# Performance work log

Hardware: AMD Instinct MI355X
Metric: run time of the kernel (lower is better)

Reference implementation:

```python
import jax, jax.numpy as jnp
import numpy as np

MARGIN = 0.1   # init kwarg m
EPS = 1e-6     # CosineSimilarity eps
B, D, C = 8192, 1024, 14
LABEL_P = 0.1


def setup_inputs() -> dict:
    key = jax.random.key(0)
    k1, k2 = jax.random.split(key)
    pred = jax.random.normal(k1, (B, D), dtype=jnp.float32)
    gt = (jax.random.uniform(k2, (B, C)) < LABEL_P).astype(jnp.float32)
    return {"pred": pred, "gt": gt}


def _cos(x, y):
    # torch.nn.CosineSimilarity(dim=1, eps=1e-6): dot / max(||x||*||y||, eps)
    dot = jnp.sum(x * y, axis=1)
    nx = jnp.sqrt(jnp.sum(x * x, axis=1))
    ny = jnp.sqrt(jnp.sum(y * y, axis=1))
    return dot / jnp.maximum(nx * ny, EPS)


def reference(pred, gt):
    n = pred.shape[0]
    has = jnp.sum(gt, axis=1) > 0                      # [B] labeled rows (idxs_a)
    share = (gt @ gt.T) > 0                            # [B,B] rows sharing any label
    # Labeled anchor: positives = rows sharing a label (incl. self),
    #                 negatives = setdiff(idxs_a, rows_pos) U idxs_n == ~share row.
    # Unlabeled anchor: positives = unlabeled rows, negatives = labeled rows.
    pos_mask = jnp.where(has[:, None], share, ~has[None, :])
    neg_mask = jnp.where(has[:, None], ~share, has[None, :])
    # Uniform sampling among masked columns via Gumbel-max (replaces random.sample)
    kp, kn = jax.random.split(jax.random.key(42))
    NEG_INF = jnp.float32(-1e30)
    pos_idx = jnp.argmax(jnp.where(pos_mask, jax.random.gumbel(kp, (n, n)), NEG_INF), axis=1)
    neg_idx = jnp.argmax(jnp.where(neg_mask, jax.random.gumbel(kn, (n, n)), NEG_INF), axis=1)
    anchor = pred
    positive = pred[pos_idx]
    negative = pred[neg_idx]
    cos_v = _cos(anchor, positive) - _cos(anchor, negative) + MARGIN
    return jnp.mean(jnp.maximum(cos_v, 0.0))
```

## Files before the change

### kernel.cpp

```cpp
#include <hip/hip_runtime.h>
#include <hip/hip_bf16.h>
#include <stdint.h>

#define NB 8192
#define ND 1024
#define NC 14

#define ROTL(x, r) __builtin_amdgcn_alignbit((x), (x), 32u - (r))
#define ADD3_IMM(x, s, imm) \
  asm("v_add3_u32 %0, %1, %2, " #imm : "=v"(x) : "v"(x), "v"(s))

static inline uint32_t rotl32h(uint32_t x, int r) { return (x << r) | (x >> (32 - r)); }
static void tf2x32_host(uint32_t k0, uint32_t k1, uint32_t x0, uint32_t x1,
                        uint32_t* o0, uint32_t* o1) {
  uint32_t ks[3] = { k0, k1, k0 ^ k1 ^ 0x1BD11BDAu };
  static const int R[8] = {13, 15, 26, 6, 17, 29, 16, 24};
  x0 += k0; x1 += k1;
  for (int g = 0; g < 5; ++g) {
    const int* rr = (g & 1) ? (R + 4) : R;
    for (int i = 0; i < 4; ++i) { x0 += x1; x1 = rotl32h(x1, rr[i]); x1 ^= x0; }
    x0 += ks[(g + 1) % 3];
    x1 += ks[(g + 2) % 3] + (uint32_t)(g + 1);
  }
  *o0 = x0; *o1 = x1;
}

__global__ void k_norm(const float* __restrict__ pred, const float* __restrict__ gt,
                       float* __restrict__ norm, uint32_t* __restrict__ lbits2) {
  const int row = blockIdx.x;
  const float4* p = (const float4*)(pred + (size_t)row * ND);
  float4 v = p[threadIdx.x];
  float s = v.x * v.x + v.y * v.y + v.z * v.z + v.w * v.w;
#pragma unroll
  for (int o = 32; o > 0; o >>= 1) s += __shfl_down(s, o, 64);
  __shared__ float red[4];
  const int wave = threadIdx.x >> 6, lane = threadIdx.x & 63;
  if (lane == 0) red[wave] = s;
  unsigned long long b =
      __ballot((int)threadIdx.x < NC && gt[row * NC + (int)threadIdx.x] != 0.0f);
  __syncthreads();
  if (threadIdx.x == 0) {
    uint32_t m = (uint32_t)(b & 0x3FFFull);
    lbits2[row] = m | ((m == 0u) ? 0x4000u : 0u);
    norm[row] = sqrtf(red[0] + red[1] + red[2] + red[3]);
  }
}

__global__ void __launch_bounds__(256) k_sample(
    const uint32_t* __restrict__ lbits2,
    uint32_t kp0, uint32_t kp1, uint32_t kps2,
    uint32_t kn0, uint32_t kn1, uint32_t kns2,
    int* __restrict__ pos_idx, int* __restrict__ neg_idx) {
  const uint32_t tid = threadIdx.x;
  const int i = blockIdx.x;
  const uint32_t bi = lbits2[i];
  const uint32_t fkp1 = kp1 + ((uint32_t)i << 13);
  const uint32_t fkn1 = kn1 + ((uint32_t)i << 13);

  uint32_t bkP = 0u, bjP = 0u, bkN = 0u, bjN = 0u;

#pragma unroll 8
  for (uint32_t k = 0; k < 32; ++k) {
    const uint32_t jv = tid + (k << 8);
    const uint32_t bj = lbits2[jv];
    const uint32_t m = bi & bj;
    const uint32_t s0 = m ? kp0 : kn0;
    const uint32_t s1 = m ? kp1 : kn1;
    const uint32_t s2 = m ? kps2 : kns2;
    const uint32_t f1 = m ? fkp1 : fkn1;
    uint32_t x0 = s0;
    uint32_t x1 = f1 + jv;
#define TFR(r) { x0 += x1; x1 = ROTL(x1, r); x1 ^= x0; }
    TFR(13) TFR(15) TFR(26) TFR(6)
    x0 += s1;  ADD3_IMM(x1, s2, 1);
    TFR(17) TFR(29) TFR(16) TFR(24)
    x0 += s2;  ADD3_IMM(x1, s0, 2);
    TFR(13) TFR(15) TFR(26) TFR(6)
    x0 += s0;  ADD3_IMM(x1, s1, 3);
    TFR(17) TFR(29) TFR(16) TFR(24)
    x0 += s1;  ADD3_IMM(x1, s2, 4);
    TFR(13) TFR(15) TFR(26) TFR(6)
    x0 += s2;  ADD3_IMM(x1, s0, 5);
#undef TFR
    const uint32_t key = (x0 ^ x1) >> 9;
    const bool pos = (m != 0u);
    const bool gtP = pos & (key > bkP);
    bkP = gtP ? key : bkP;
    bjP = gtP ? jv : bjP;
    const bool gtN = (!pos) & (key > bkN);
    bkN = gtN ? key : bkN;
    bjN = gtN ? jv : bjN;
  }

#pragma unroll
  for (int off = 32; off > 0; off >>= 1) {
    uint32_t k2 = __shfl_down(bkP, off, 64), j2 = __shfl_down(bjP, off, 64);
    if (k2 > bkP || (k2 == bkP && j2 < bjP)) { bkP = k2; bjP = j2; }
    k2 = __shfl_down(bkN, off, 64); j2 = __shfl_down(bjN, off, 64);
    if (k2 > bkN || (k2 == bkN && j2 < bjN)) { bkN = k2; bjN = j2; }
  }
  __shared__ uint32_t sk[2][4], sj[2][4];
  const int wave = (int)tid >> 6, lane = (int)tid & 63;
  if (lane == 0) { sk[0][wave] = bkP; sj[0][wave] = bjP; sk[1][wave] = bkN; sj[1][wave] = bjN; }
  __syncthreads();
  if (tid == 0) {
    uint32_t bk = sk[0][0], bj = sj[0][0];
#pragma unroll
    for (int w = 1; w < 4; ++w)
      if (sk[0][w] > bk || (sk[0][w] == bk && sj[0][w] < bj)) { bk = sk[0][w]; bj = sj[0][w]; }
    pos_idx[i] = (int)bj;
    bk = sk[1][0]; bj = sj[1][0];
#pragma unroll
    for (int w = 1; w < 4; ++w)
      if (sk[1][w] > bk || (sk[1][w] == bk && sj[1][w] < bj)) { bk = sk[1][w]; bj = sj[1][w]; }
    neg_idx[i] = (int)bj;
  }
}

__global__ void k_loss(const float* __restrict__ pred, const float* __restrict__ norm,
                       const int* __restrict__ pos_idx, const int* __restrict__ neg_idx,
                       float* __restrict__ losses) {
  const int i = blockIdx.x;
  const int p = pos_idx[i];
  const int n = neg_idx[i];
  const float4* A = (const float4*)(pred + (size_t)i * ND);
  const float4* P = (const float4*)(pred + (size_t)p * ND);
  const float4* Nn = (const float4*)(pred + (size_t)n * ND);
  float4 a = A[threadIdx.x], pp = P[threadIdx.x], nn = Nn[threadIdx.x];
  float dp = a.x * pp.x + a.y * pp.y + a.z * pp.z + a.w * pp.w;
  float dn = a.x * nn.x + a.y * nn.y + a.z * nn.z + a.w * nn.w;
#pragma unroll
  for (int o = 32; o > 0; o >>= 1) {
    dp += __shfl_down(dp, o, 64);
    dn += __shfl_down(dn, o, 64);
  }
  __shared__ float rdp[4], rdn[4];
  int wave = threadIdx.x >> 6, lane = threadIdx.x & 63;
  if (lane == 0) { rdp[wave] = dp; rdn[wave] = dn; }
  __syncthreads();
  if (threadIdx.x == 0) {
    float DP = rdp[0] + rdp[1] + rdp[2] + rdp[3];
    float DN = rdn[0] + rdn[1] + rdn[2] + rdn[3];
    float na = norm[i];
    float cp = DP / fmaxf(na * norm[p], 1e-6f);
    float cn = DN / fmaxf(na * norm[n], 1e-6f);
    losses[i] = fmaxf(cp - cn + 0.1f, 0.0f);
  }
}

__global__ void k_mean(const float* __restrict__ losses, float* __restrict__ out) {
  float s = 0.0f;
  for (int k = threadIdx.x; k < NB; k += 256) s += losses[k];
#pragma unroll
  for (int o = 32; o > 0; o >>= 1) s += __shfl_down(s, o, 64);
  __shared__ float red[4];
  int wave = threadIdx.x >> 6, lane = threadIdx.x & 63;
  if (lane == 0) red[wave] = s;
  __syncthreads();
  if (threadIdx.x == 0) out[0] = (red[0] + red[1] + red[2] + red[3]) / (float)NB;
}

extern "C" void kernel_launch(void* const* d_in, const int* in_sizes, int n_in,
                              void* d_out, int out_size, void* d_ws, size_t ws_size,
                              hipStream_t stream) {
  const float* pred = (const float*)d_in[0];
  const float* gt   = (const float*)d_in[1];
  float* out = (float*)d_out;

  char* ws = (char*)d_ws;
  uint32_t* lbits = (uint32_t*)(ws);
  float*    norms = (float*)(ws + 32768);
  int*      posi  = (int*)(ws + 65536);
  int*      negi  = (int*)(ws + 98304);
  float*    losses= (float*)(ws + 131072);

  uint32_t kp0, kp1, kn0, kn1;
  tf2x32_host(0u, 42u, 0u, 0u, &kp0, &kp1);
  tf2x32_host(0u, 42u, 0u, 1u, &kn0, &kn1);
  const uint32_t kps2 = kp0 ^ kp1 ^ 0x1BD11BDAu;
  const uint32_t kns2 = kn0 ^ kn1 ^ 0x1BD11BDAu;

  k_norm<<<NB, 256, 0, stream>>>(pred, gt, norms, lbits);
  k_sample<<<NB, 256, 0, stream>>>(lbits, kp0, kp1, kps2, kn0, kn1, kns2, posi, negi);
  k_loss<<<NB, 256, 0, stream>>>(pred, norms, posi, negi, losses);
  k_mean<<<1, 256, 0, stream>>>(losses, out);
}
```

Baseline: 242.0 us.

## Fuse sampling with loss, compute norms inline, and pack argmax keys

Replaces the per-row norm kernel with a small labels-only kernel that handles 256 rows per block. Fuses Gumbel sampling and the loss into one kernel that recomputes the anchor, positive and negative norms from the rows it already loads. The sampling loop now packs the key and the loop index into one word, so the running max needs no separate index compare. This removes a full 32MB pass over pred, two launches and the index round-trips through global memory, at the cost of extra FMAs and shuffles per block.

```diff
diff --git a/kernel.cpp b/kernel.cpp
--- a/kernel.cpp
+++ b/kernel.cpp
@@ -25,51 +25,37 @@
   *o0 = x0; *o1 = x1;
 }
 
-__global__ void k_norm(const float* __restrict__ pred, const float* __restrict__ gt,
-                       float* __restrict__ norm, uint32_t* __restrict__ lbits2) {
-  const int row = blockIdx.x;
-  const float4* p = (const float4*)(pred + (size_t)row * ND);
-  float4 v = p[threadIdx.x];
-  float s = v.x * v.x + v.y * v.y + v.z * v.z + v.w * v.w;
+__global__ void k_labels(const float* __restrict__ gt, uint32_t* __restrict__ lbits2) {
+  const int i = blockIdx.x * 256 + threadIdx.x;
+  uint32_t m = 0u;
 #pragma unroll
-  for (int o = 32; o > 0; o >>= 1) s += __shfl_down(s, o, 64);
-  __shared__ float red[4];
-  const int wave = threadIdx.x >> 6, lane = threadIdx.x & 63;
-  if (lane == 0) red[wave] = s;
-  unsigned long long b =
-      __ballot((int)threadIdx.x < NC && gt[row * NC + (int)threadIdx.x] != 0.0f);
-  __syncthreads();
-  if (threadIdx.x == 0) {
-    uint32_t m = (uint32_t)(b & 0x3FFFull);
-    lbits2[row] = m | ((m == 0u) ? 0x4000u : 0u);
-    norm[row] = sqrtf(red[0] + red[1] + red[2] + red[3]);
-  }
+  for (int c = 0; c < NC; ++c)
+    m |= (gt[i * NC + c] != 0.0f) ? (1u << c) : 0u;
+  lbits2[i] = m ? m : 0x4000u;
 }
 
-__global__ void __launch_bounds__(256) k_sample(
-    const uint32_t* __restrict__ lbits2,
+__global__ void __launch_bounds__(256) k_fused(
+    const uint32_t* __restrict__ lbits2, const float* __restrict__ pred,
     uint32_t kp0, uint32_t kp1, uint32_t kps2,
     uint32_t kn0, uint32_t kn1, uint32_t kns2,
-    int* __restrict__ pos_idx, int* __restrict__ neg_idx) {
+    float* __restrict__ losses) {
   const uint32_t tid = threadIdx.x;
   const int i = blockIdx.x;
   const uint32_t bi = lbits2[i];
-  const uint32_t fkp1 = kp1 + ((uint32_t)i << 13);
-  const uint32_t fkn1 = kn1 + ((uint32_t)i << 13);
+  const uint32_t ftP = kp1 + ((uint32_t)i << 13) + tid;
+  const uint32_t ftN = kn1 + ((uint32_t)i << 13) + tid;
 
-  uint32_t bkP = 0u, bjP = 0u, bkN = 0u, bjN = 0u;
+  uint32_t bkP = 0u, bkN = 0u;
 
 #pragma unroll 8
   for (uint32_t k = 0; k < 32; ++k) {
-    const uint32_t jv = tid + (k << 8);
-    const uint32_t bj = lbits2[jv];
+    const uint32_t bj = lbits2[tid + (k << 8)];
     const uint32_t m = bi & bj;
     const uint32_t s0 = m ? kp0 : kn0;
     const uint32_t s1 = m ? kp1 : kn1;
     const uint32_t s2 = m ? kps2 : kns2;
-    const uint32_t f1 = m ? fkp1 : fkn1;
     uint32_t x0 = s0;
-    uint32_t x1 = f1 + jv;
+    uint32_t x1 = (m ? ftP : ftN) + (k << 8);
 #define TFR(r) { x0 += x1; x1 = ROTL(x1, r); x1 ^= x0; }
     TFR(13) TFR(15) TFR(26) TFR(6)
     x0 += s1;  ADD3_IMM(x1, s2, 1);
@@ -82,68 +68,73 @@
     TFR(13) TFR(15) TFR(26) TFR(6)
     x0 += s2;  ADD3_IMM(x1, s0, 5);
 #undef TFR
-    const uint32_t key = (x0 ^ x1) >> 9;
-    const bool pos = (m != 0u);
-    const bool gtP = pos & (key > bkP);
-    bkP = gtP ? key : bkP;
-    bjP = gtP ? jv : bjP;
-    const bool gtN = (!pos) & (key > bkN);
-    bkN = gtN ? key : bkN;
-    bjN = gtN ? jv : bjN;
+    const uint32_t t = x0 ^ x1;
+    const uint32_t cand = ((t >> 9) << 5) + (31u - k);
+    const uint32_t selP = m ? cand : 0u;
+    const uint32_t selN = cand ^ selP;
+    bkP = bkP > selP ? bkP : selP;
+    bkN = bkN > selN ? bkN : selN;
   }
 
+  uint32_t keyP = bkP >> 5, jP = tid + ((31u - (bkP & 31u)) << 8);
+  uint32_t keyN = bkN >> 5, jN = tid + ((31u - (bkN & 31u)) << 8);
 #pragma unroll
   for (int off = 32; off > 0; off >>= 1) {
-    uint32_t k2 = __shfl_down(bkP, off, 64), j2 = __shfl_down(bjP, off, 64);
-    if (k2 > bkP || (k2 == bkP && j2 < bjP)) { bkP = k2; bjP = j2; }
-    k2 = __shfl_down(bkN, off, 64); j2 = __shfl_down(bjN, off, 64);
-    if (k2 > bkN || (k2 == bkN && j2 < bjN)) { bkN = k2; bjN = j2; }
+    uint32_t k2 = __shfl_down(keyP, off, 64), j2 = __shfl_down(jP, off, 64);
+    if (k2 > keyP || (k2 == keyP && j2 < jP)) { keyP = k2; jP = j2; }
+    k2 = __shfl_down(keyN, off, 64); j2 = __shfl_down(jN, off, 64);
+    if (k2 > keyN || (k2 == keyN && j2 < jN)) { keyN = k2; jN = j2; }
   }
   __shared__ uint32_t sk[2][4], sj[2][4];
+  __shared__ int spn[2];
   const int wave = (int)tid >> 6, lane = (int)tid & 63;
-  if (lane == 0) { sk[0][wave] = bkP; sj[0][wave] = bjP; sk[1][wave] = bkN; sj[1][wave] = bjN; }
+  if (lane == 0) { sk[0][wave] = keyP; sj[0][wave] = jP; sk[1][wave] = keyN; sj[1][wave] = jN; }
   __syncthreads();
   if (tid == 0) {
     uint32_t bk = sk[0][0], bj = sj[0][0];
 #pragma unroll
     for (int w = 1; w < 4; ++w)
       if (sk[0][w] > bk || (sk[0][w] == bk && sj[0][w] < bj)) { bk = sk[0][w]; bj = sj[0][w]; }
-    pos_idx[i] = (int)bj;
+    spn[0] = (int)bj;
     bk = sk[1][0]; bj = sj[1][0];
 #pragma unroll
     for (int w = 1; w < 4; ++w)
       if (sk[1][w] > bk || (sk[1][w] == bk && sj[1][w] < bj)) { bk = sk[1][w]; bj = sj[1][w]; }
-    neg_idx[i] = (int)bj;
+    spn[1] = (int)bj;
   }
-}
+  __syncthreads();
 
-__global__ void k_loss(const float* __restrict__ pred, const float* __restrict__ norm,
-                       const int* __restrict__ pos_idx, const int* __restrict__ neg_idx,
-                       float* __restrict__ losses) {
-  const int i = blockIdx.x;
-  const int p = pos_idx[i];
-  const int n = neg_idx[i];
-  const float4* A = (const float4*)(pred + (size_t)i * ND);
-  const float4* P = (const float4*)(pred + (size_t)p * ND);
-  const float4* Nn = (const float4*)(pred + (size_t)n * ND);
-  float4 a = A[threadIdx.x], pp = P[threadIdx.x], nn = Nn[threadIdx.x];
-  float dp = a.x * pp.x + a.y * pp.y + a.z * pp.z + a.w * pp.w;
-  float dn = a.x * nn.x + a.y * nn.y + a.z * nn.z + a.w * nn.w;
+  const int p = spn[0], n = spn[1];
+  const float4* A  = (const float4*)(pred + (size_t)i * ND);
+  const float4* P  = (const float4*)(pred + (size_t)p * ND);
+  const float4* Nv = (const float4*)(pred + (size_t)n * ND);
+  float4 a = A[tid], pv = P[tid], nv = Nv[tid];
+  float na = a.x * a.x + a.y * a.y + a.z * a.z + a.w * a.w;
+  float np = pv.x * pv.x + pv.y * pv.y + pv.z * pv.z + pv.w * pv.w;
+  float nn = nv.x * nv.x + nv.y * nv.y + nv.z * nv.z + nv.w * nv.w;
+  float dp = a.x * pv.x + a.y * pv.y + a.z * pv.z + a.w * pv.w;
+  float dn = a.x * nv.x + a.y * nv.y + a.z * nv.z + a.w * nv.w;
 #pragma unroll
   for (int o = 32; o > 0; o >>= 1) {
+    na += __shfl_down(na, o, 64);
+    np += __shfl_down(np, o, 64);
+    nn += __shfl_down(nn, o, 64);
     dp += __shfl_down(dp, o, 64);
     dn += __shfl_down(dn, o, 64);
   }
-  __shared__ float rdp[4], rdn[4];
-  int wave = threadIdx.x >> 6, lane = threadIdx.x & 63;
-  if (lane == 0) { rdp[wave] = dp; rdn[wave] = dn; }
+  __shared__ float red[4][5];
+  if (lane == 0) { red[wave][0] = na; red[wave][1] = np; red[wave][2] = nn;
+                   red[wave][3] = dp; red[wave][4] = dn; }
   __syncthreads();
-  if (threadIdx.x == 0) {
-    float DP = rdp[0] + rdp[1] + rdp[2] + rdp[3];
-    float DN = rdn[0] + rdn[1] + rdn[2] + rdn[3];
-    float na = norm[i];
-    float cp = DP / fmaxf(na * norm[p], 1e-6f);
-    float cn = DN / fmaxf(na * norm[n], 1e-6f);
+  if (tid == 0) {
+    float NA = red[0][0] + red[1][0] + red[2][0] + red[3][0];
+    float NP = red[0][1] + red[1][1] + red[2][1] + red[3][1];
+    float NN = red[0][2] + red[1][2] + red[2][2] + red[3][2];
+    float DP = red[0][3] + red[1][3] + red[2][3] + red[3][3];
+    float DN = red[0][4] + red[1][4] + red[2][4] + red[3][4];
+    NA = sqrtf(NA); NP = sqrtf(NP); NN = sqrtf(NN);
+    float cp = DP / fmaxf(NA * NP, 1e-6f);
+    float cn = DN / fmaxf(NA * NN, 1e-6f);
     losses[i] = fmaxf(cp - cn + 0.1f, 0.0f);
   }
 }
@@ -168,11 +159,8 @@
   float* out = (float*)d_out;
 
   char* ws = (char*)d_ws;
-  uint32_t* lbits = (uint32_t*)(ws);
-  float*    norms = (float*)(ws + 32768);
-  int*      posi  = (int*)(ws + 65536);
-  int*      negi  = (int*)(ws + 98304);
-  float*    losses= (float*)(ws + 131072);
+  uint32_t* lbits  = (uint32_t*)(ws);
+  float*    losses = (float*)(ws + 32768);
 
   uint32_t kp0, kp1, kn0, kn1;
   tf2x32_host(0u, 42u, 0u, 0u, &kp0, &kp1);
@@ -180,8 +168,7 @@
   const uint32_t kps2 = kp0 ^ kp1 ^ 0x1BD11BDAu;
   const uint32_t kns2 = kn0 ^ kn1 ^ 0x1BD11BDAu;
 
-  k_norm<<<NB, 256, 0, stream>>>(pred, gt, norms, lbits);
-  k_sample<<<NB, 256, 0, stream>>>(lbits, kp0, kp1, kps2, kn0, kn1, kns2, posi, negi);
-  k_loss<<<NB, 256, 0, stream>>>(pred, norms, posi, negi, losses);
+  k_labels<<<NB / 256, 256, 0, stream>>>(gt, lbits);
+  k_fused<<<NB, 256, 0, stream>>>(lbits, pred, kp0, kp1, kps2, kn0, kn1, kns2, losses);
   k_mean<<<1, 256, 0, stream>>>(losses, out);
 }
```

After: 229.1 us. -5.3%, faster.
